# Kernel tuning notes

Measured on AMD Instinct MI355X. Metric: run time of the kernel, lower is better.

## Reference

```python
import jax, jax.numpy as jnp
import numpy as np


def setup_inputs() -> dict:
    key = jax.random.key(0)
    k1, k2 = jax.random.split(key)
    n, m, d = 8192, 8192, 64
    x = jax.random.normal(k1, (n, d), dtype=jnp.float32)
    y = jax.random.normal(k2, (m, d), dtype=jnp.float32)
    gamma = jnp.ones((), dtype=jnp.float32)  # learnable bandwidth, init_gamma=1.0
    return {"x": x, "y": y, "gamma": gamma}


def reference(x, y, gamma):
    # RBF kernel: exp(-gamma * ||x_i - y_j||^2), computed via the
    x_sq = jnp.sum(x * x, axis=-1, keepdims=True)          # (n, 1)
    y_sq = jnp.sum(y * y, axis=-1, keepdims=True).T        # (1, m)
    xy = x @ y.T                                           # (n, m) GEMM
    sq_dist = jnp.maximum(x_sq + y_sq - 2.0 * xy, 0.0)     # clamp fp error
    return jnp.exp(-gamma * sq_dist)                       # (n, m)
```

## Files before the change

### kernel.cpp

```cpp
#include <hip/hip_runtime.h>
#include <hip/hip_bf16.h>


#define DD 64
#define BM 128
#define BN 128

typedef __attribute__((ext_vector_type(8))) short short8;
typedef __attribute__((ext_vector_type(4))) float f32x4;

#if __has_builtin(__builtin_amdgcn_exp2f)
#define EXP2(x) __builtin_amdgcn_exp2f(x)
#else
#define EXP2(x) exp2f(x)
#endif

__device__ __forceinline__ unsigned short f2bf_rne(float f) {
  unsigned u = __float_as_uint(f);
  unsigned r = u + 0x7FFFu + ((u >> 16) & 1u);
  return (unsigned short)(r >> 16);
}

__global__ __launch_bounds__(256)
void prep_split(const float* __restrict__ X, const float* __restrict__ Y,
                unsigned short* __restrict__ XHg, unsigned short* __restrict__ XLg,
                unsigned short* __restrict__ YHg, unsigned short* __restrict__ YLg,
                float* __restrict__ xsq, float* __restrict__ ysq, int n) {
  int t = blockIdx.x * 256 + threadIdx.x;
  int row = t >> 4;
  int c4 = t & 15;
  const float* src;
  unsigned short *hd, *ld;
  float* nd;
  int r;
  if (row < n) { r = row;     src = X + (long)r * DD; hd = XHg; ld = XLg; nd = xsq + r; }
  else         { r = row - n; src = Y + (long)r * DD; hd = YHg; ld = YLg; nd = ysq + r; }
  float4 v = ((const float4*)src)[c4];
  float f[4] = {v.x, v.y, v.z, v.w};
  unsigned short h[4], l[4];
#pragma unroll
  for (int q = 0; q < 4; ++q) {
    h[q] = f2bf_rne(f[q]);
    float hv = __uint_as_float(((unsigned)h[q]) << 16);
    l[q] = f2bf_rne(f[q] - hv);
  }
  int sw = (c4 * 8) ^ ((r & 7) << 4);
  *(ushort4*)((char*)hd + (long)r * 128 + sw) = make_ushort4(h[0], h[1], h[2], h[3]);
  *(ushort4*)((char*)ld + (long)r * 128 + sw) = make_ushort4(l[0], l[1], l[2], l[3]);
  float s = v.x * v.x + v.y * v.y + v.z * v.z + v.w * v.w;
  s += __shfl_xor(s, 1);
  s += __shfl_xor(s, 2);
  s += __shfl_xor(s, 4);
  s += __shfl_xor(s, 8);
  if (c4 == 0) *nd = s;
}

__global__ __launch_bounds__(256, 2)
void rbf_fence(const unsigned short* __restrict__ XHg, const unsigned short* __restrict__ XLg,
               const unsigned short* __restrict__ YHg, const unsigned short* __restrict__ YLg,
               const float* __restrict__ gptr,
               const float* __restrict__ xsq, const float* __restrict__ ysq,
               float* __restrict__ Out, int mcols) {
  __shared__ __align__(128) char lds[65536];

  const int tid = threadIdx.x;
  const int lane = tid & 63;
  const int wid = tid >> 6;
  const long i0 = (long)blockIdx.y * BM;
  const long j0 = (long)blockIdx.x * BN;

  const char* srcs[4] = {(const char*)XHg + i0 * 128, (const char*)XLg + i0 * 128,
                         (const char*)YHg + j0 * 128, (const char*)YLg + j0 * 128};
#pragma unroll
  for (int t4 = 0; t4 < 4; ++t4) {
#pragma unroll
    for (int it = 0; it < 4; ++it) {
      int off = it * 4096 + wid * 1024;
      const char* g = srcs[t4] + off + lane * 16;
      __builtin_amdgcn_global_load_lds(
          (const __attribute__((address_space(1))) void*)g,
          (__attribute__((address_space(3))) void*)(lds + t4 * 16384 + off),
          16, 0, 0);
    }
  }
  __syncthreads();

  const int wr = wid >> 1, wc = wid & 1;
  const int lr = lane & 15;
  const int hg = lane >> 4;

  short8 afh[2][4], afl[2][4];
  short8 bfh[2][4], bfl[2][4];
#pragma unroll
  for (int s = 0; s < 2; ++s)
#pragma unroll
    for (int q = 0; q < 4; ++q) {
      int ra = wr * 64 + q * 16 + lr;
      int oa = (s * 64 + hg * 16) ^ ((ra & 7) << 4);
      afh[s][q] = *(const short8*)(lds + ra * 128 + oa);
      afl[s][q] = *(const short8*)(lds + 16384 + ra * 128 + oa);
      int rb = wc * 64 + q * 16 + lr;
      int ob = (s * 64 + hg * 16) ^ ((rb & 7) << 4);
      bfh[s][q] = *(const short8*)(lds + 32768 + rb * 128 + ob);
      bfl[s][q] = *(const short8*)(lds + 49152 + rb * 128 + ob);
    }

  const float g = *gptr;
  const float cf = -g * 1.4426950408889634f;
  const float nc2 = -2.0f * cf;
  float cxr[4];
#pragma unroll
  for (int m2 = 0; m2 < 4; ++m2) cxr[m2] = cf * xsq[i0 + wr * 64 + m2 * 16 + lr];
  float4 cyv[4];
#pragma unroll
  for (int n2 = 0; n2 < 4; ++n2) {
    float4 yq = *(const float4*)&ysq[j0 + wc * 64 + n2 * 16 + hg * 4];
    cyv[n2] = make_float4(cf * yq.x, cf * yq.y, cf * yq.z, cf * yq.w);
  }

#pragma unroll
  for (int m2 = 0; m2 < 4; ++m2) {
    long row = i0 + wr * 64 + m2 * 16 + lr;
    float* op = Out + row * (long)mcols + j0 + wc * 64 + hg * 4;
#pragma unroll
    for (int n2 = 0; n2 < 4; ++n2) {
      f32x4 acc = (f32x4){0.f, 0.f, 0.f, 0.f};
#pragma unroll
      for (int s = 0; s < 2; ++s) {
        acc = __builtin_amdgcn_mfma_f32_16x16x32_bf16(bfh[s][n2], afh[s][m2], acc, 0, 0, 0);
        acc = __builtin_amdgcn_mfma_f32_16x16x32_bf16(bfh[s][n2], afl[s][m2], acc, 0, 0, 0);
        acc = __builtin_amdgcn_mfma_f32_16x16x32_bf16(bfl[s][n2], afh[s][m2], acc, 0, 0, 0);
      }
      float cy[4] = {cyv[n2].x, cyv[n2].y, cyv[n2].z, cyv[n2].w};
      float o[4];
#pragma unroll
      for (int j = 0; j < 4; ++j)
        o[j] = EXP2(fminf(fmaf(nc2, acc[j], cxr[m2] + cy[j]), 0.f));
      *(float4*)(op + n2 * 16) = *(float4*)o;
      __builtin_amdgcn_sched_barrier(0);
    }
  }
}

__global__ __launch_bounds__(256)
void prep_sq(const float* __restrict__ X, const float* __restrict__ Y,
             float* __restrict__ xsq, float* __restrict__ ysq, int n) {
  int t = blockIdx.x * 256 + threadIdx.x;
  int row = t >> 4;
  int c = t & 15;
  const float* src;
  float* dst;
  if (row < n) { src = X + (long)row * DD; dst = xsq + row; }
  else         { src = Y + (long)(row - n) * DD; dst = ysq + (row - n); }
  float4 v = ((const float4*)src)[c];
  float s = v.x * v.x + v.y * v.y + v.z * v.z + v.w * v.w;
  s += __shfl_xor(s, 1);
  s += __shfl_xor(s, 2);
  s += __shfl_xor(s, 4);
  s += __shfl_xor(s, 8);
  if (c == 0) *dst = s;
}

__global__ __launch_bounds__(256, 2)
void rbf_mfma_fb(const float* __restrict__ X, const float* __restrict__ Y,
                 const float* __restrict__ gptr,
                 const float* __restrict__ xsq, const float* __restrict__ ysq,
                 float* __restrict__ Out, int mcols) {
  __shared__ unsigned short XH[128 * DD], XL[128 * DD];
  __shared__ unsigned short YH[128 * DD], YL[128 * DD];
  const int tid = threadIdx.x;
  const long i0 = (long)blockIdx.y * 128;
  const long j0 = (long)blockIdx.x * 128;
#pragma unroll
  for (int it = 0; it < 16; ++it) {
    int e = it * 256 + tid;
    int half = e >> 11;
    int idx = e & 2047;
    int row = idx >> 4;
    int c4 = idx & 15;
    const float* src = half ? (Y + (j0 + row) * DD) : (X + (i0 + row) * DD);
    float4 v = ((const float4*)src)[c4];
    float f[4] = {v.x, v.y, v.z, v.w};
    unsigned short h[4], l[4];
#pragma unroll
    for (int q = 0; q < 4; ++q) {
      h[q] = f2bf_rne(f[q]);
      float hv = __uint_as_float(((unsigned)h[q]) << 16);
      l[q] = f2bf_rne(f[q] - hv);
    }
    int sw = (c4 * 8) ^ ((row & 7) << 4);
    unsigned short* Ht = half ? YH : XH;
    unsigned short* Lt = half ? YL : XL;
    *(ushort4*)((char*)Ht + row * 128 + sw) = make_ushort4(h[0], h[1], h[2], h[3]);
    *(ushort4*)((char*)Lt + row * 128 + sw) = make_ushort4(l[0], l[1], l[2], l[3]);
  }
  __syncthreads();
  const int lane = tid & 63;
  const int wid = tid >> 6;
  const int wr = wid >> 1, wc = wid & 1;
  const int lr = lane & 15;
  const int hg = lane >> 4;
  f32x4 acc[4][4];
#pragma unroll
  for (int a = 0; a < 4; ++a)
#pragma unroll
    for (int c = 0; c < 4; ++c) acc[a][c] = (f32x4){0.f, 0.f, 0.f, 0.f};
  const unsigned short* At[3] = {XH, XL, XH};
  const unsigned short* Bt[3] = {YH, YH, YL};
#pragma unroll
  for (int p = 0; p < 3; ++p) {
#pragma unroll
    for (int s = 0; s < 2; ++s) {
      const int kbyte = s * 64 + hg * 16;
      short8 af[4], bfv[4];
#pragma unroll
      for (int m2 = 0; m2 < 4; ++m2) {
        int row = wr * 64 + m2 * 16 + lr;
        af[m2] = *(const short8*)((const char*)At[p] + row * 128 + (kbyte ^ ((row & 7) << 4)));
      }
#pragma unroll
      for (int n2 = 0; n2 < 4; ++n2) {
        int row = wc * 64 + n2 * 16 + lr;
        bfv[n2] = *(const short8*)((const char*)Bt[p] + row * 128 + (kbyte ^ ((row & 7) << 4)));
      }
#pragma unroll
      for (int m2 = 0; m2 < 4; ++m2)
#pragma unroll
        for (int n2 = 0; n2 < 4; ++n2)
          acc[m2][n2] = __builtin_amdgcn_mfma_f32_16x16x32_bf16(af[m2], bfv[n2], acc[m2][n2], 0, 0, 0);
    }
  }
  const float g = *gptr;
  float yv[4];
#pragma unroll
  for (int n2 = 0; n2 < 4; ++n2) yv[n2] = ysq[j0 + wc * 64 + n2 * 16 + lr];
#pragma unroll
  for (int m2 = 0; m2 < 4; ++m2) {
#pragma unroll
    for (int j = 0; j < 4; ++j) {
      long row = i0 + wr * 64 + m2 * 16 + hg * 4 + j;
      float xr = xsq[row];
      float* op = Out + row * (long)mcols + j0 + wc * 64 + lr;
#pragma unroll
      for (int n2 = 0; n2 < 4; ++n2) {
        float d = fmaxf(xr + yv[n2] - 2.0f * acc[m2][n2][j], 0.f);
        op[n2 * 16] = __expf(-g * d);
      }
    }
  }
}

extern "C" void kernel_launch(void* const* d_in, const int* in_sizes, int n_in,
                              void* d_out, int out_size, void* d_ws, size_t ws_size,
                              hipStream_t stream) {
  const float* x = (const float*)d_in[0];
  const float* y = (const float*)d_in[1];
  const float* g = (const float*)d_in[2];
  float* out = (float*)d_out;

  const int n = in_sizes[0] / DD;
  const int m = in_sizes[1] / DD;

  const size_t split_bytes = (size_t)(n + m) * DD * 2 * sizeof(unsigned short);
  const size_t needed = split_bytes + (size_t)(n + m) * sizeof(float);

  if (ws_size >= needed && (n % BM) == 0 && (m % BN) == 0) {
    unsigned short* XHg = (unsigned short*)d_ws;
    unsigned short* XLg = XHg + (size_t)n * DD;
    unsigned short* YHg = XLg + (size_t)n * DD;
    unsigned short* YLg = YHg + (size_t)m * DD;
    float* xsq = (float*)(YLg + (size_t)m * DD);
    float* ysq = xsq + n;
    prep_split<<<(n + m) / 16, 256, 0, stream>>>(x, y, XHg, XLg, YHg, YLg, xsq, ysq, n);
    dim3 grid(m / BN, n / BM);
    rbf_fence<<<grid, 256, 0, stream>>>(XHg, XLg, YHg, YLg, g, xsq, ysq, out, m);
  } else {
    float* xsq = (float*)d_ws;
    float* ysq = xsq + n;
    prep_sq<<<(n + m) / 16, 256, 0, stream>>>(x, y, xsq, ysq, n);
    dim3 grid2(m / 128, n / 128);
    rbf_mfma_fb<<<grid2, 256, 0, stream>>>(x, y, g, xsq, ysq, out, m);
  }
}
```

Measured before the change: 56.17 us.

## Overlap low-part tile loads with high-part MFMAs via partial vmcnt wait

Reorders the global-to-LDS loads so the high bf16 halves of X and Y are issued first. The kernel then waits only for those (vmcnt(8)) and runs the hi*hi MFMAs across all 16 output tiles while the low halves are still in flight. After a full barrier it loads the low halves and finishes the hi*lo and lo*hi terms before the exp and store epilogue. The aim is to hide load latency behind compute, at the cost of a 64-register accumulator array held live across the barrier, which raises register pressure and could hurt occupancy at 2 blocks per CU.

```diff
diff --git a/kernel.cpp b/kernel.cpp
--- a/kernel.cpp
+++ b/kernel.cpp
@@ -56,11 +56,11 @@
 }
 
 __global__ __launch_bounds__(256, 2)
-void rbf_fence(const unsigned short* __restrict__ XHg, const unsigned short* __restrict__ XLg,
-               const unsigned short* __restrict__ YHg, const unsigned short* __restrict__ YLg,
-               const float* __restrict__ gptr,
-               const float* __restrict__ xsq, const float* __restrict__ ysq,
-               float* __restrict__ Out, int mcols) {
+void rbf_pipe(const unsigned short* __restrict__ XHg, const unsigned short* __restrict__ XLg,
+              const unsigned short* __restrict__ YHg, const unsigned short* __restrict__ YLg,
+              const float* __restrict__ gptr,
+              const float* __restrict__ xsq, const float* __restrict__ ysq,
+              float* __restrict__ Out, int mcols) {
   __shared__ __align__(128) char lds[65536];
 
   const int tid = threadIdx.x;
@@ -69,8 +69,11 @@
   const long i0 = (long)blockIdx.y * BM;
   const long j0 = (long)blockIdx.x * BN;
 
-  const char* srcs[4] = {(const char*)XHg + i0 * 128, (const char*)XLg + i0 * 128,
-                         (const char*)YHg + j0 * 128, (const char*)YLg + j0 * 128};
+  const char* srcs[4] = {(const char*)XHg + i0 * 128,
+                         (const char*)YHg + j0 * 128,
+                         (const char*)XLg + i0 * 128,
+                         (const char*)YLg + j0 * 128};
+  const int dsts[4] = {0, 32768, 16384, 49152};
 #pragma unroll
   for (int t4 = 0; t4 < 4; ++t4) {
 #pragma unroll
@@ -79,18 +82,19 @@
       const char* g = srcs[t4] + off + lane * 16;
       __builtin_amdgcn_global_load_lds(
           (const __attribute__((address_space(1))) void*)g,
-          (__attribute__((address_space(3))) void*)(lds + t4 * 16384 + off),
+          (__attribute__((address_space(3))) void*)(lds + dsts[t4] + off),
           16, 0, 0);
     }
   }
-  __syncthreads();
+
+  asm volatile("s_waitcnt vmcnt(8)" ::: "memory");
+  __builtin_amdgcn_s_barrier();
 
   const int wr = wid >> 1, wc = wid & 1;
   const int lr = lane & 15;
   const int hg = lane >> 4;
 
-  short8 afh[2][4], afl[2][4];
-  short8 bfh[2][4], bfl[2][4];
+  short8 afh[2][4], bfh[2][4];
 #pragma unroll
   for (int s = 0; s < 2; ++s)
 #pragma unroll
@@ -98,11 +102,9 @@
       int ra = wr * 64 + q * 16 + lr;
       int oa = (s * 64 + hg * 16) ^ ((ra & 7) << 4);
       afh[s][q] = *(const short8*)(lds + ra * 128 + oa);
-      afl[s][q] = *(const short8*)(lds + 16384 + ra * 128 + oa);
       int rb = wc * 64 + q * 16 + lr;
       int ob = (s * 64 + hg * 16) ^ ((rb & 7) << 4);
       bfh[s][q] = *(const short8*)(lds + 32768 + rb * 128 + ob);
-      bfl[s][q] = *(const short8*)(lds + 49152 + rb * 128 + ob);
     }
 
   const float g = *gptr;
@@ -118,24 +120,52 @@
     cyv[n2] = make_float4(cf * yq.x, cf * yq.y, cf * yq.z, cf * yq.w);
   }
 
+  f32x4 acc[4][4];
+#pragma unroll
+  for (int a = 0; a < 4; ++a)
+#pragma unroll
+    for (int c = 0; c < 4; ++c) acc[a][c] = (f32x4){0.f, 0.f, 0.f, 0.f};
+
+#pragma unroll
+  for (int s = 0; s < 2; ++s)
+#pragma unroll
+    for (int m2 = 0; m2 < 4; ++m2)
+#pragma unroll
+      for (int n2 = 0; n2 < 4; ++n2)
+        acc[m2][n2] = __builtin_amdgcn_mfma_f32_16x16x32_bf16(bfh[s][n2], afh[s][m2], acc[m2][n2], 0, 0, 0);
+
+  __syncthreads();
+
+  short8 afl[2][4], bfl[2][4];
+#pragma unroll
+  for (int s = 0; s < 2; ++s)
+#pragma unroll
+    for (int q = 0; q < 4; ++q) {
+      int ra = wr * 64 + q * 16 + lr;
+      int oa = (s * 64 + hg * 16) ^ ((ra & 7) << 4);
+      afl[s][q] = *(const short8*)(lds + 16384 + ra * 128 + oa);
+      int rb = wc * 64 + q * 16 + lr;
+      int ob = (s * 64 + hg * 16) ^ ((rb & 7) << 4);
+      bfl[s][q] = *(const short8*)(lds + 49152 + rb * 128 + ob);
+    }
+
 #pragma unroll
   for (int m2 = 0; m2 < 4; ++m2) {
     long row = i0 + wr * 64 + m2 * 16 + lr;
     float* op = Out + row * (long)mcols + j0 + wc * 64 + hg * 4;
 #pragma unroll
     for (int n2 = 0; n2 < 4; ++n2) {
-      f32x4 acc = (f32x4){0.f, 0.f, 0.f, 0.f};
+      f32x4 a = acc[m2][n2];
 #pragma unroll
       for (int s = 0; s < 2; ++s) {
-        acc = __builtin_amdgcn_mfma_f32_16x16x32_bf16(bfh[s][n2], afh[s][m2], acc, 0, 0, 0);
-        acc = __builtin_amdgcn_mfma_f32_16x16x32_bf16(bfh[s][n2], afl[s][m2], acc, 0, 0, 0);
-        acc = __builtin_amdgcn_mfma_f32_16x16x32_bf16(bfl[s][n2], afh[s][m2], acc, 0, 0, 0);
+        a = __builtin_amdgcn_mfma_f32_16x16x32_bf16(bfh[s][n2], afl[s][m2], a, 0, 0, 0);
+        a = __builtin_amdgcn_mfma_f32_16x16x32_bf16(bfl[s][n2], afh[s][m2], a, 0, 0, 0);
       }
       float cy[4] = {cyv[n2].x, cyv[n2].y, cyv[n2].z, cyv[n2].w};
       float o[4];
 #pragma unroll
       for (int j = 0; j < 4; ++j)
-        o[j] = EXP2(fminf(fmaf(nc2, acc[j], cxr[m2] + cy[j]), 0.f));
+        o[j] = EXP2(fminf(fmaf(nc2, a[j], cxr[m2] + cy[j]), 0.f));
       *(float4*)(op + n2 * 16) = *(float4*)o;
       __builtin_amdgcn_sched_barrier(0);
     }
@@ -273,7 +303,7 @@
     float* ysq = xsq + n;
     prep_split<<<(n + m) / 16, 256, 0, stream>>>(x, y, XHg, XLg, YHg, YLg, xsq, ysq, n);
     dim3 grid(m / BN, n / BM);
-    rbf_fence<<<grid, 256, 0, stream>>>(XHg, XLg, YHg, YLg, g, xsq, ysq, out, m);
+    rbf_pipe<<<grid, 256, 0, stream>>>(XHg, XLg, YHg, YLg, g, xsq, ysq, out, m);
   } else {
     float* xsq = (float*)d_ws;
     float* ysq = xsq + n;
```

After: 57.81 us. +2.9%, slower.

## Process two column tiles per block and prefetch second Y tile during first

Applied to the files above, without the earlier changes.

Each block now computes two adjacent 128-column output tiles, halving the grid. The X fragments stay in registers across both tiles. The second tile's Y hi/lo data is loaded into LDS asynchronously while the first tile's MFMA, exp and store work runs. This aims to cut per-block launch and X reload overhead and to hide the Y load latency. In exchange there are fewer blocks, a hand-written vmcnt wait that depends on the exact count of outstanding memory operations, and a stricter divisibility condition on m.

```diff
diff --git a/kernel.cpp b/kernel.cpp
--- a/kernel.cpp
+++ b/kernel.cpp
@@ -56,18 +56,18 @@
 }
 
 __global__ __launch_bounds__(256, 2)
-void rbf_fence(const unsigned short* __restrict__ XHg, const unsigned short* __restrict__ XLg,
-               const unsigned short* __restrict__ YHg, const unsigned short* __restrict__ YLg,
-               const float* __restrict__ gptr,
-               const float* __restrict__ xsq, const float* __restrict__ ysq,
-               float* __restrict__ Out, int mcols) {
+void rbf_2t(const unsigned short* __restrict__ XHg, const unsigned short* __restrict__ XLg,
+            const unsigned short* __restrict__ YHg, const unsigned short* __restrict__ YLg,
+            const float* __restrict__ gptr,
+            const float* __restrict__ xsq, const float* __restrict__ ysq,
+            float* __restrict__ Out, int mcols) {
   __shared__ __align__(128) char lds[65536];
 
   const int tid = threadIdx.x;
   const int lane = tid & 63;
   const int wid = tid >> 6;
   const long i0 = (long)blockIdx.y * BM;
-  const long j0 = (long)blockIdx.x * BN;
+  const long j0 = (long)blockIdx.x * (2 * BN);
 
   const char* srcs[4] = {(const char*)XHg + i0 * 128, (const char*)XLg + i0 * 128,
                          (const char*)YHg + j0 * 128, (const char*)YLg + j0 * 128};
@@ -76,9 +76,9 @@
 #pragma unroll
     for (int it = 0; it < 4; ++it) {
       int off = it * 4096 + wid * 1024;
-      const char* g = srcs[t4] + off + lane * 16;
+      const char* gp = srcs[t4] + off + lane * 16;
       __builtin_amdgcn_global_load_lds(
-          (const __attribute__((address_space(1))) void*)g,
+          (const __attribute__((address_space(1))) void*)gp,
           (__attribute__((address_space(3))) void*)(lds + t4 * 16384 + off),
           16, 0, 0);
     }
@@ -111,33 +111,97 @@
   float cxr[4];
 #pragma unroll
   for (int m2 = 0; m2 < 4; ++m2) cxr[m2] = cf * xsq[i0 + wr * 64 + m2 * 16 + lr];
-  float4 cyv[4];
-#pragma unroll
-  for (int n2 = 0; n2 < 4; ++n2) {
-    float4 yq = *(const float4*)&ysq[j0 + wc * 64 + n2 * 16 + hg * 4];
-    cyv[n2] = make_float4(cf * yq.x, cf * yq.y, cf * yq.z, cf * yq.w);
-  }
-
-#pragma unroll
-  for (int m2 = 0; m2 < 4; ++m2) {
-    long row = i0 + wr * 64 + m2 * 16 + lr;
-    float* op = Out + row * (long)mcols + j0 + wc * 64 + hg * 4;
+
+  __syncthreads();
+
+  {
+    const char* yh = (const char*)YHg + (j0 + BN) * 128;
+    const char* yl = (const char*)YLg + (j0 + BN) * 128;
+#pragma unroll
+    for (int it = 0; it < 4; ++it) {
+      int off = it * 4096 + wid * 1024;
+      __builtin_amdgcn_global_load_lds(
+          (const __attribute__((address_space(1))) void*)(yh + off + lane * 16),
+          (__attribute__((address_space(3))) void*)(lds + 32768 + off), 16, 0, 0);
+      __builtin_amdgcn_global_load_lds(
+          (const __attribute__((address_space(1))) void*)(yl + off + lane * 16),
+          (__attribute__((address_space(3))) void*)(lds + 49152 + off), 16, 0, 0);
+    }
+  }
+
+  {
+    float4 cyv[4];
 #pragma unroll
     for (int n2 = 0; n2 < 4; ++n2) {
-      f32x4 acc = (f32x4){0.f, 0.f, 0.f, 0.f};
-#pragma unroll
-      for (int s = 0; s < 2; ++s) {
-        acc = __builtin_amdgcn_mfma_f32_16x16x32_bf16(bfh[s][n2], afh[s][m2], acc, 0, 0, 0);
-        acc = __builtin_amdgcn_mfma_f32_16x16x32_bf16(bfh[s][n2], afl[s][m2], acc, 0, 0, 0);
-        acc = __builtin_amdgcn_mfma_f32_16x16x32_bf16(bfl[s][n2], afh[s][m2], acc, 0, 0, 0);
-      }
-      float cy[4] = {cyv[n2].x, cyv[n2].y, cyv[n2].z, cyv[n2].w};
-      float o[4];
-#pragma unroll
-      for (int j = 0; j < 4; ++j)
-        o[j] = EXP2(fminf(fmaf(nc2, acc[j], cxr[m2] + cy[j]), 0.f));
-      *(float4*)(op + n2 * 16) = *(float4*)o;
-      __builtin_amdgcn_sched_barrier(0);
+      float4 yq = *(const float4*)&ysq[j0 + wc * 64 + n2 * 16 + hg * 4];
+      cyv[n2] = make_float4(cf * yq.x, cf * yq.y, cf * yq.z, cf * yq.w);
+    }
+#pragma unroll
+    for (int m2 = 0; m2 < 4; ++m2) {
+      long row = i0 + wr * 64 + m2 * 16 + lr;
+      float* op = Out + row * (long)mcols + j0 + wc * 64 + hg * 4;
+#pragma unroll
+      for (int n2 = 0; n2 < 4; ++n2) {
+        f32x4 a = (f32x4){0.f, 0.f, 0.f, 0.f};
+#pragma unroll
+        for (int s = 0; s < 2; ++s) {
+          a = __builtin_amdgcn_mfma_f32_16x16x32_bf16(bfh[s][n2], afh[s][m2], a, 0, 0, 0);
+          a = __builtin_amdgcn_mfma_f32_16x16x32_bf16(bfh[s][n2], afl[s][m2], a, 0, 0, 0);
+          a = __builtin_amdgcn_mfma_f32_16x16x32_bf16(bfl[s][n2], afh[s][m2], a, 0, 0, 0);
+        }
+        float o[4];
+        o[0] = EXP2(fminf(fmaf(nc2, a[0], cxr[m2] + cyv[n2].x), 0.f));
+        o[1] = EXP2(fminf(fmaf(nc2, a[1], cxr[m2] + cyv[n2].y), 0.f));
+        o[2] = EXP2(fminf(fmaf(nc2, a[2], cxr[m2] + cyv[n2].z), 0.f));
+        o[3] = EXP2(fminf(fmaf(nc2, a[3], cxr[m2] + cyv[n2].w), 0.f));
+        *(float4*)(op + n2 * 16) = *(float4*)o;
+        __builtin_amdgcn_sched_barrier(0);
+      }
+    }
+  }
+
+  asm volatile("s_waitcnt vmcnt(16)" ::: "memory");
+  __builtin_amdgcn_s_barrier();
+
+#pragma unroll
+  for (int s = 0; s < 2; ++s)
+#pragma unroll
+    for (int q = 0; q < 4; ++q) {
+      int rb = wc * 64 + q * 16 + lr;
+      int ob = (s * 64 + hg * 16) ^ ((rb & 7) << 4);
+      bfh[s][q] = *(const short8*)(lds + 32768 + rb * 128 + ob);
+      bfl[s][q] = *(const short8*)(lds + 49152 + rb * 128 + ob);
+    }
+
+  {
+    const long j1 = j0 + BN;
+    float4 cyv[4];
+#pragma unroll
+    for (int n2 = 0; n2 < 4; ++n2) {
+      float4 yq = *(const float4*)&ysq[j1 + wc * 64 + n2 * 16 + hg * 4];
+      cyv[n2] = make_float4(cf * yq.x, cf * yq.y, cf * yq.z, cf * yq.w);
+    }
+#pragma unroll
+    for (int m2 = 0; m2 < 4; ++m2) {
+      long row = i0 + wr * 64 + m2 * 16 + lr;
+      float* op = Out + row * (long)mcols + j1 + wc * 64 + hg * 4;
+#pragma unroll
+      for (int n2 = 0; n2 < 4; ++n2) {
+        f32x4 a = (f32x4){0.f, 0.f, 0.f, 0.f};
+#pragma unroll
+        for (int s = 0; s < 2; ++s) {
+          a = __builtin_amdgcn_mfma_f32_16x16x32_bf16(bfh[s][n2], afh[s][m2], a, 0, 0, 0);
+          a = __builtin_amdgcn_mfma_f32_16x16x32_bf16(bfh[s][n2], afl[s][m2], a, 0, 0, 0);
+          a = __builtin_amdgcn_mfma_f32_16x16x32_bf16(bfl[s][n2], afh[s][m2], a, 0, 0, 0);
+        }
+        float o[4];
+        o[0] = EXP2(fminf(fmaf(nc2, a[0], cxr[m2] + cyv[n2].x), 0.f));
+        o[1] = EXP2(fminf(fmaf(nc2, a[1], cxr[m2] + cyv[n2].y), 0.f));
+        o[2] = EXP2(fminf(fmaf(nc2, a[2], cxr[m2] + cyv[n2].z), 0.f));
+        o[3] = EXP2(fminf(fmaf(nc2, a[3], cxr[m2] + cyv[n2].w), 0.f));
+        *(float4*)(op + n2 * 16) = *(float4*)o;
+        __builtin_amdgcn_sched_barrier(0);
+      }
     }
   }
 }
@@ -264,7 +328,7 @@
   const size_t split_bytes = (size_t)(n + m) * DD * 2 * sizeof(unsigned short);
   const size_t needed = split_bytes + (size_t)(n + m) * sizeof(float);
 
-  if (ws_size >= needed && (n % BM) == 0 && (m % BN) == 0) {
+  if (ws_size >= needed && (n % BM) == 0 && (m % (2 * BN)) == 0) {
     unsigned short* XHg = (unsigned short*)d_ws;
     unsigned short* XLg = XHg + (size_t)n * DD;
     unsigned short* YHg = XLg + (size_t)n * DD;
@@ -272,8 +336,8 @@
     float* xsq = (float*)(YLg + (size_t)m * DD);
     float* ysq = xsq + n;
     prep_split<<<(n + m) / 16, 256, 0, stream>>>(x, y, XHg, XLg, YHg, YLg, xsq, ysq, n);
-    dim3 grid(m / BN, n / BM);
-    rbf_fence<<<grid, 256, 0, stream>>>(XHg, XLg, YHg, YLg, g, xsq, ysq, out, m);
+    dim3 grid(m / (2 * BN), n / BM);
+    rbf_2t<<<grid, 256, 0, stream>>>(XHg, XLg, YHg, YLg, g, xsq, ysq, out, m);
   } else {
     float* xsq = (float*)d_ws;
     float* ysq = xsq + n;
```

New measurement: 54.49 us. 3.0% less time.
